# Performance work log

Measured on AMD Instinct MI355X. Metric: run time of the kernel, lower is better.

The kernel has to match this reference:

```python
import jax, jax.numpy as jnp
import numpy as np

B, S, H, I, SI, E, TOPK = 2, 1024, 1024, 512, 2048, 8, 2


def setup_inputs() -> dict:
    key = jax.random.key(0)
    ks = jax.random.split(key, 8)
    w = 0.02
    return {
        "hidden_states": jax.random.normal(ks[0], (B, S, H), jnp.float32),
        "router_weight": jax.random.normal(ks[1], (E, H), jnp.float32) * w,
        "gate_up_proj": jax.random.normal(ks[2], (E, 2 * I, H), jnp.float32) * w,
        "down_proj": jax.random.normal(ks[3], (E, H, I), jnp.float32) * w,
        "shared_gate_w": jax.random.normal(ks[4], (SI, H), jnp.float32) * w,
        "shared_up_w": jax.random.normal(ks[5], (SI, H), jnp.float32) * w,
        "shared_down_w": jax.random.normal(ks[6], (H, SI), jnp.float32) * w,
        "shared_expert_gate_w": jax.random.normal(ks[7], (1, H), jnp.float32) * w,
    }


def reference(hidden_states, router_weight, gate_up_proj, down_proj,
              shared_gate_w, shared_up_w, shared_down_w, shared_expert_gate_w):
    b, s, h = hidden_states.shape
    x = hidden_states.reshape(-1, h)  # [T, H]

    # shared expert (SwiGLU)
    shared = (jax.nn.silu(x @ shared_gate_w.T) * (x @ shared_up_w.T)) @ shared_down_w.T  # [T, H]

    # top-k softmax router (softmax in fp32, renormalized top-k weights)
    logits = x @ router_weight.T  # [T, E]
    probs = jax.nn.softmax(logits.astype(jnp.float32), axis=-1)
    top_v, top_i = jax.lax.top_k(probs, TOPK)
    top_v = (top_v / jnp.sum(top_v, axis=-1, keepdims=True)).astype(logits.dtype)  # [T, K]

    # combine weights per (token, expert): sum over k of routing weight * one_hot
    cw = jnp.sum(jax.nn.one_hot(top_i, E, dtype=top_v.dtype) * top_v[..., None], axis=1)  # [T, E]

    # grouped-expert SwiGLU (dense compute, masked combine == gather/scatter math)
    gu = jnp.einsum('th,eih->eti', x, gate_up_proj)  # [E, T, 2I]
    gate, up = jnp.split(gu, 2, axis=-1)
    act = jax.nn.silu(gate) * up  # [E, T, I]
    per_expert = jnp.einsum('eti,ehi->eth', act, down_proj)  # [E, T, H]
    expert_out = jnp.einsum('eth,te->th', per_expert, cw)  # [T, H]

    out = expert_out + jax.nn.sigmoid(x @ shared_expert_gate_w.T) * shared
    return out.reshape(b, s, h)
```

## Files before the change

kernel.cpp:

```cpp
#include <hip/hip_runtime.h>

#define T_TOK 2048
#define H_DIM 1024
#define I_DIM 512
#define SI_DIM 2048
#define E_NUM 8
#define NSLOT 4096

typedef __attribute__((ext_vector_type(8))) short short8;
typedef __attribute__((ext_vector_type(4))) float floatx4;

__device__ inline unsigned short f2bf(float f) {
  unsigned u = __builtin_bit_cast(unsigned, f);
  u = (u + 0x7FFFu + ((u >> 16) & 1u)) >> 16;
  return (unsigned short)u;
}
__device__ inline float bf2f(unsigned short u) {
  return __builtin_bit_cast(float, (unsigned)u << 16);
}

__device__ inline void gl_lds16(const void* g, void* l) {
  __builtin_amdgcn_global_load_lds(
      (const __attribute__((address_space(1))) unsigned int*)g,
      (__attribute__((address_space(3))) unsigned int*)l, 16, 0, 0);
}

__global__ __launch_bounds__(256) void cast_router(
    const float* __restrict__ x, const float* __restrict__ rw,
    const float* __restrict__ segw,
    const float* __restrict__ s1, const float* __restrict__ s2,
    const float* __restrict__ s3, const float* __restrict__ s4,
    const float* __restrict__ s5,
    unsigned short* __restrict__ d0, unsigned short* __restrict__ d1,
    unsigned short* __restrict__ d2, unsigned short* __restrict__ d3,
    unsigned short* __restrict__ d4, unsigned short* __restrict__ d5,
    int* __restrict__ top2, float2* __restrict__ w01, float* __restrict__ sg) {
  const int bid = blockIdx.x;
  if (bid < 512) {
    int t = bid * 4 + (threadIdx.x >> 6);
    int lane = threadIdx.x & 63;
    const float* xt = x + (long)t * H_DIM;
    float xv[16];
#pragma unroll
    for (int j = 0; j < 16; ++j) xv[j] = xt[j * 64 + lane];
    float dots[9];
#pragma unroll
    for (int e = 0; e < 8; ++e) {
      const float* w = rw + e * H_DIM;
      float s = 0.f;
#pragma unroll
      for (int j = 0; j < 16; ++j) s += xv[j] * w[j * 64 + lane];
      dots[e] = s;
    }
    {
      float s = 0.f;
#pragma unroll
      for (int j = 0; j < 16; ++j) s += xv[j] * segw[j * 64 + lane];
      dots[8] = s;
    }
#pragma unroll
    for (int off = 32; off > 0; off >>= 1) {
#pragma unroll
      for (int e = 0; e < 9; ++e) dots[e] += __shfl_xor(dots[e], off, 64);
    }
    if (lane == 0) {
      int e0 = 0;
      for (int e = 1; e < 8; ++e)
        if (dots[e] > dots[e0]) e0 = e;
      int e1 = (e0 == 0) ? 1 : 0;
      for (int e = 0; e < 8; ++e)
        if (e != e0 && dots[e] > dots[e1]) e1 = e;
      float p1 = expf(dots[e1] - dots[e0]);
      top2[t] = e0 | (e1 << 8);
      w01[t] = make_float2(1.f / (1.f + p1), p1 / (1.f + p1));
      sg[t] = 1.f / (1.f + expf(-dots[8]));
    }
  } else {
    long g = (long)(bid - 512) * 256 + threadIdx.x;
    const float* s;
    unsigned short* d;
    long off;
    if (g < 524288L)       { s = x;  d = d0; off = g; }
    else if (g < 2621440L) { s = s1; d = d1; off = g - 524288L; }
    else if (g < 3670016L) { s = s2; d = d2; off = g - 2621440L; }
    else if (g < 4194304L) { s = s3; d = d3; off = g - 3670016L; }
    else if (g < 4718592L) { s = s4; d = d4; off = g - 4194304L; }
    else                   { s = s5; d = d5; off = g - 4718592L; }
    float4 v = ((const float4*)s)[off];
    ushort4 o;
    o.x = f2bf(v.x); o.y = f2bf(v.y); o.z = f2bf(v.z); o.w = f2bf(v.w);
    ((ushort4*)d)[off] = o;
  }
}

__global__ __launch_bounds__(256) void build_lists(
    const int* __restrict__ top2, int* __restrict__ cnt, int* __restrict__ ebase,
    int* __restrict__ slot_token, int* __restrict__ tok_slot) {
  const int e = blockIdx.x;
  const int tid = threadIdx.x;
  const int lane = tid & 63, wid = tid >> 6;
  __shared__ int wsum[4], wbelow[4];
  const int base_t = tid * 8;
  int mk[8], kk[8];
  int c = 0, below = 0;
#pragma unroll
  for (int j = 0; j < 8; ++j) {
    int p = top2[base_t + j];
    int e0 = p & 0xFF, e1 = (p >> 8) & 0xFF;
    below += (e0 < e) + (e1 < e);
    int m = 0, k = 0;
    if (e0 == e) { m = 1; k = 0; }
    else if (e1 == e) { m = 1; k = 1; }
    mk[j] = m; kk[j] = k;
    c += m;
  }
  int inc = c;
#pragma unroll
  for (int off = 1; off < 64; off <<= 1) {
    int n = __shfl_up(inc, off, 64);
    if (lane >= off) inc += n;
  }
  int bsum = below;
#pragma unroll
  for (int off = 32; off > 0; off >>= 1) bsum += __shfl_xor(bsum, off, 64);
  if (lane == 63) wsum[wid] = inc;
  if (lane == 0) wbelow[wid] = bsum;
  __syncthreads();
  int woff = 0;
#pragma unroll
  for (int i = 0; i < 4; ++i)
    if (i < wid) woff += wsum[i];
  int baseE = wbelow[0] + wbelow[1] + wbelow[2] + wbelow[3];
  int pos = baseE + woff + inc - c;
#pragma unroll
  for (int j = 0; j < 8; ++j) {
    if (mk[j]) {
      slot_token[pos] = base_t + j;
      tok_slot[2 * (base_t + j) + kk[j]] = pos;
      pos++;
    }
  }
  if (tid == 255) cnt[e] = woff + inc;
  if (tid == 0) ebase[e] = baseE;
}

template <bool GATHER>
__device__ __forceinline__ void swiglu_body(
    char* smem, int bx, int by, int e,
    const unsigned short* __restrict__ A, const unsigned short* __restrict__ Bg,
    const unsigned short* __restrict__ Bu, unsigned short* __restrict__ Out,
    const int* __restrict__ slot_token, const int* __restrict__ cnt,
    const int* __restrict__ ebase, int N, int K, long estrideB) {
  constexpr int BM = 128, BN = 128, BK = 32;
  constexpr int ATILE = BM * BK;
  constexpr int BTILE = BN * BK;
  const int tid = threadIdx.x;
  const int lane = tid & 63;
  const int wid = tid >> 6;
  const int wm = wid & 1;
  const int wn = wid >> 1;
  const int m0 = by * BM;
  const int n0 = bx * BN;
  int Meff = 0, baseE = 0;
  if (GATHER) {
    Meff = cnt[e];
    if (m0 >= Meff) return;
    baseE = ebase[e];
  }
  const unsigned short* BgE = Bg + (long)e * estrideB;
  const unsigned short* BuE = Bu + (long)e * estrideB;

  unsigned short* As = (unsigned short*)smem;
  unsigned short* Bgs = As + 2 * ATILE;
  unsigned short* Bus = Bgs + 2 * BTILE;

  const int lrow = lane >> 2;
  const int lcol = (((lane & 3) ^ ((lrow >> 1) & 3)) << 4);

  const char* aP[2];
  const char* bgP[2];
  const char* buP[2];
#pragma unroll
  for (int i = 0; i < 2; ++i) {
    int m = m0 + wid * 32 + i * 16 + lrow;
    long row;
    if (GATHER) {
      int mm = (m < Meff - 1) ? m : (Meff - 1);
      row = slot_token[baseE + mm];
    } else {
      row = m;
    }
    aP[i] = (const char*)A + row * (long)(K * 2) + lcol;
    int n = n0 + wid * 32 + i * 16 + lrow;
    bgP[i] = (const char*)BgE + (long)n * (K * 2) + lcol;
    buP[i] = (const char*)BuE + (long)n * (K * 2) + lcol;
  }

  floatx4 accG[4][4], accU[4][4];
  floatx4 zero = {0.f, 0.f, 0.f, 0.f};
#pragma unroll
  for (int i = 0; i < 4; ++i)
#pragma unroll
    for (int j = 0; j < 4; ++j) { accG[i][j] = zero; accU[i][j] = zero; }

  const int ar = lane & 15;
  const int aksw = (((lane >> 4) ^ ((ar >> 1) & 3)) << 3);

  auto stage = [&](int p, int k0) {
#pragma unroll
    for (int i = 0; i < 2; ++i) {
      gl_lds16(aP[i] + (long)k0 * 2, &As[p * ATILE + (wid * 32 + i * 16) * BK]);
      gl_lds16(bgP[i] + (long)k0 * 2, &Bgs[p * BTILE + (wid * 32 + i * 16) * BK]);
      gl_lds16(buP[i] + (long)k0 * 2, &Bus[p * BTILE + (wid * 32 + i * 16) * BK]);
    }
  };

  stage(0, 0);
  const int NI = K / BK;
  for (int i = 0; i < NI; ++i) {
    __syncthreads();
    if (i + 1 < NI) stage((i + 1) & 1, (i + 1) * BK);
    const unsigned short* Ab = &As[(i & 1) * ATILE];
    const unsigned short* Gb = &Bgs[(i & 1) * BTILE];
    const unsigned short* Ub = &Bus[(i & 1) * BTILE];
    short8 af[4], bgf[4], buf2[4];
#pragma unroll
    for (int tm = 0; tm < 4; ++tm)
      af[tm] = *(const short8*)&Ab[(wm * 64 + tm * 16 + ar) * BK + aksw];
#pragma unroll
    for (int tn = 0; tn < 4; ++tn) {
      bgf[tn] = *(const short8*)&Gb[(wn * 64 + tn * 16 + ar) * BK + aksw];
      buf2[tn] = *(const short8*)&Ub[(wn * 64 + tn * 16 + ar) * BK + aksw];
    }
#pragma unroll
    for (int tm = 0; tm < 4; ++tm)
#pragma unroll
      for (int tn = 0; tn < 4; ++tn) {
        accG[tm][tn] = __builtin_amdgcn_mfma_f32_16x16x32_bf16(af[tm], bgf[tn], accG[tm][tn], 0, 0, 0);
        accU[tm][tn] = __builtin_amdgcn_mfma_f32_16x16x32_bf16(af[tm], buf2[tn], accU[tm][tn], 0, 0, 0);
      }
  }

#pragma unroll
  for (int tm = 0; tm < 4; ++tm)
#pragma unroll
    for (int tn = 0; tn < 4; ++tn)
#pragma unroll
      for (int r = 0; r < 4; ++r) {
        int row = m0 + wm * 64 + tm * 16 + (lane >> 4) * 4 + r;
        int col = n0 + wn * 64 + tn * 16 + (lane & 15);
        if (!GATHER || row < Meff) {
          float g = accG[tm][tn][r];
          float u = accU[tm][tn][r];
          float act = g / (1.f + expf(-g)) * u;
          Out[(long)(baseE + row) * N + col] = f2bf(act);
        }
      }
}

__global__ __launch_bounds__(256, 2) void swiglu_fused(
    const unsigned short* __restrict__ xb, const unsigned short* __restrict__ sgate,
    const unsigned short* __restrict__ sup, unsigned short* __restrict__ act_s,
    const unsigned short* __restrict__ gup, unsigned short* __restrict__ act_e,
    const int* __restrict__ slot_token, const int* __restrict__ cnt,
    const int* __restrict__ ebase) {
  __shared__ __align__(16) char smem[49152];
  int bid = blockIdx.x;
  if (bid < 256) {
    swiglu_body<false>(smem, bid & 15, bid >> 4, 0, xb, sgate, sup, act_s,
                       nullptr, nullptr, nullptr, SI_DIM, H_DIM, 0);
  } else {
    int b2 = bid - 256;
    int e = b2 >> 6;
    int rem = b2 & 63;
    swiglu_body<true>(smem, rem & 3, rem >> 2, e, xb, gup,
                      gup + (long)I_DIM * H_DIM, act_e, slot_token, cnt,
                      ebase, I_DIM, H_DIM, (long)2 * I_DIM * H_DIM);
  }
}

template <int MODE>
__device__ __forceinline__ void down_body(
    char* smem, int bx, int by, int e,
    const unsigned short* __restrict__ A, const unsigned short* __restrict__ B,
    float* __restrict__ OutF, unsigned short* __restrict__ OutB,
    const int* __restrict__ ebase, const int* __restrict__ cnt,
    int N, int Kstride, int kbeg, int kcnt, long estrideB) {
  constexpr int BM = 128, BN = 256, BK = 32;
  constexpr int ATILE = BM * BK;
  constexpr int BTILE = BN * BK;
  const int tid = threadIdx.x;
  const int lane = tid & 63;
  const int wid = tid >> 6;
  const int wm = wid & 1;
  const int wn = wid >> 1;
  const int m0 = by * BM;
  const int n0 = bx * BN;
  int Meff = 0, baseE = 0;
  if (MODE == 1) {
    Meff = cnt[e];
    if (m0 >= Meff) return;
    baseE = ebase[e];
  }
  const unsigned short* BE = B + (long)e * estrideB;

  unsigned short* As = (unsigned short*)smem;
  unsigned short* Bs = As + 2 * ATILE;

  const int lrow = lane >> 2;
  const int lcol = (((lane & 3) ^ ((lrow >> 1) & 3)) << 4);

  const char* aP[2];
  const char* bP[4];
#pragma unroll
  for (int i = 0; i < 2; ++i) {
    int m = m0 + wid * 32 + i * 16 + lrow;
    long arow;
    if (MODE == 1) {
      int mm = (m < Meff - 1) ? m : (Meff - 1);
      arow = baseE + mm;
    } else {
      arow = m;
    }
    aP[i] = (const char*)A + arow * (long)(Kstride * 2) + (long)kbeg * 2 + lcol;
  }
#pragma unroll
  for (int i = 0; i < 4; ++i) {
    int n = n0 + wid * 64 + i * 16 + lrow;
    bP[i] = (const char*)BE + (long)n * (Kstride * 2) + (long)kbeg * 2 + lcol;
  }

  floatx4 acc[4][8];
  floatx4 zero = {0.f, 0.f, 0.f, 0.f};
#pragma unroll
  for (int i = 0; i < 4; ++i)
#pragma unroll
    for (int j = 0; j < 8; ++j) acc[i][j] = zero;

  const int ar = lane & 15;
  const int aksw = (((lane >> 4) ^ ((ar >> 1) & 3)) << 3);

  auto stage = [&](int p, int k0) {
#pragma unroll
    for (int i = 0; i < 2; ++i)
      gl_lds16(aP[i] + (long)k0 * 2, &As[p * ATILE + (wid * 32 + i * 16) * BK]);
#pragma unroll
    for (int i = 0; i < 4; ++i)
      gl_lds16(bP[i] + (long)k0 * 2, &Bs[p * BTILE + (wid * 64 + i * 16) * BK]);
  };

  stage(0, 0);
  const int NI = kcnt / BK;
  for (int i = 0; i < NI; ++i) {
    __syncthreads();
    if (i + 1 < NI) stage((i + 1) & 1, (i + 1) * BK);
    const unsigned short* Ab = &As[(i & 1) * ATILE];
    const unsigned short* Bb = &Bs[(i & 1) * BTILE];
    short8 af[4], bf[8];
#pragma unroll
    for (int tm = 0; tm < 4; ++tm)
      af[tm] = *(const short8*)&Ab[(wm * 64 + tm * 16 + ar) * BK + aksw];
#pragma unroll
    for (int tn = 0; tn < 8; ++tn)
      bf[tn] = *(const short8*)&Bb[(wn * 128 + tn * 16 + ar) * BK + aksw];
#pragma unroll
    for (int tm = 0; tm < 4; ++tm)
#pragma unroll
      for (int tn = 0; tn < 8; ++tn)
        acc[tm][tn] = __builtin_amdgcn_mfma_f32_16x16x32_bf16(af[tm], bf[tn], acc[tm][tn], 0, 0, 0);
  }

#pragma unroll
  for (int tm = 0; tm < 4; ++tm)
#pragma unroll
    for (int r = 0; r < 4; ++r) {
      int row = m0 + wm * 64 + tm * 16 + (lane >> 4) * 4 + r;
#pragma unroll
      for (int tn = 0; tn < 8; ++tn) {
        int col = n0 + wn * 128 + tn * 16 + (lane & 15);
        float v = acc[tm][tn][r];
        if (MODE == 0) {
          OutF[(long)row * N + col] = v;
        } else if (MODE == 2) {
          OutB[(long)row * N + col] = f2bf(v);
        } else if (row < Meff) {
          OutB[(long)(baseE + row) * N + col] = f2bf(v);
        }
      }
    }
}

__global__ __launch_bounds__(256, 2) void down_fused(
    const unsigned short* __restrict__ act_s, const unsigned short* __restrict__ sdown,
    float* __restrict__ out, unsigned short* __restrict__ spart,
    const unsigned short* __restrict__ act_e, const unsigned short* __restrict__ downw,
    unsigned short* __restrict__ eout, const int* __restrict__ ebase,
    const int* __restrict__ cnt) {
  __shared__ __align__(16) char smem[49152];
  int bid = blockIdx.x;
  if (bid < 128) {
    int ks = bid >> 6;
    int rem = bid & 63;
    if (ks == 0)
      down_body<0>(smem, rem & 3, rem >> 2, 0, act_s, sdown, out, nullptr,
                   nullptr, nullptr, H_DIM, SI_DIM, 0, 1024, 0);
    else
      down_body<2>(smem, rem & 3, rem >> 2, 0, act_s, sdown, nullptr, spart,
                   nullptr, nullptr, H_DIM, SI_DIM, 1024, 1024, 0);
  } else {
    int b2 = bid - 128;
    int e = b2 >> 6;
    int rem = b2 & 63;
    down_body<1>(smem, rem & 3, rem >> 2, e, act_e, downw, nullptr, eout,
                 ebase, cnt, H_DIM, I_DIM, 0, I_DIM, (long)H_DIM * I_DIM);
  }
}

__global__ __launch_bounds__(256) void combine_kernel(
    float* __restrict__ out, const unsigned short* __restrict__ spart,
    const unsigned short* __restrict__ eout, const float* __restrict__ sg,
    const float2* __restrict__ w01, const int* __restrict__ tok_slot) {
  int t = blockIdx.x;
  int c = threadIdx.x;
  float sgr = sg[t];
  float2 wr = w01[t];
  int s0 = tok_slot[2 * t];
  int s1 = tok_slot[2 * t + 1];
  ushort4 p1 = ((const ushort4*)(spart + (long)t * H_DIM))[c];
  ushort4 e0 = ((const ushort4*)(eout + (long)s0 * H_DIM))[c];
  ushort4 e1 = ((const ushort4*)(eout + (long)s1 * H_DIM))[c];
  float4* op = &((float4*)(out + (long)t * H_DIM))[c];
  float4 o = *op;
  o.x = sgr * (o.x + bf2f(p1.x)) + wr.x * bf2f(e0.x) + wr.y * bf2f(e1.x);
  o.y = sgr * (o.y + bf2f(p1.y)) + wr.x * bf2f(e0.y) + wr.y * bf2f(e1.y);
  o.z = sgr * (o.z + bf2f(p1.z)) + wr.x * bf2f(e0.z) + wr.y * bf2f(e1.z);
  o.w = sgr * (o.w + bf2f(p1.w)) + wr.x * bf2f(e0.w) + wr.y * bf2f(e1.w);
  *op = o;
}

extern "C" void kernel_launch(void* const* d_in, const int* in_sizes, int n_in,
                              void* d_out, int out_size, void* d_ws, size_t ws_size,
                              hipStream_t stream) {
  const float* x = (const float*)d_in[0];
  const float* rw = (const float*)d_in[1];
  const float* gup = (const float*)d_in[2];
  const float* dwn = (const float*)d_in[3];
  const float* sgw = (const float*)d_in[4];
  const float* suw = (const float*)d_in[5];
  const float* sdw = (const float*)d_in[6];
  const float* segw = (const float*)d_in[7];
  float* out = (float*)d_out;

  char* w = (char*)d_ws;
  unsigned short* xb = (unsigned short*)(w + 0);
  unsigned short* gup_b = (unsigned short*)(w + 4194304L);
  unsigned short* down_b = (unsigned short*)(w + 20971520L);
  unsigned short* sgate_b = (unsigned short*)(w + 29360128L);
  unsigned short* sup_b = (unsigned short*)(w + 33554432L);
  unsigned short* sdown_b = (unsigned short*)(w + 37748736L);
  unsigned short* act_s = (unsigned short*)(w + 41943040L);
  unsigned short* act_e = (unsigned short*)(w + 50331648L);
  unsigned short* eout = (unsigned short*)(w + 54525952L);
  float* sg = (float*)(w + 62914560L);
  int* top2 = (int*)(w + 62922752L);
  float2* w01 = (float2*)(w + 62930944L);
  int* cnt = (int*)(w + 62947328L);
  int* ebase = (int*)(w + 62947584L);
  int* slot_token = (int*)(w + 62947840L);
  int* tok_slot = (int*)(w + 62964224L);
  unsigned short* spart = xb;

  cast_router<<<20992, 256, 0, stream>>>(x, rw, segw, gup, dwn, sgw, suw, sdw,
                                         xb, gup_b, down_b, sgate_b, sup_b,
                                         sdown_b, top2, w01, sg);
  build_lists<<<E_NUM, 256, 0, stream>>>(top2, cnt, ebase, slot_token, tok_slot);
  swiglu_fused<<<768, 256, 0, stream>>>(xb, sgate_b, sup_b, act_s, gup_b,
                                        act_e, slot_token, cnt, ebase);
  down_fused<<<640, 256, 0, stream>>>(act_s, sdown_b, out, spart, act_e,
                                      down_b, eout, ebase, cnt);
  combine_kernel<<<T_TOK, 256, 0, stream>>>(out, spart, eout, sg, w01, tok_slot);
}
```

Before: 200.2 us.

## Fuse combine into down GEMM epilogue via scaled atomicAdd into zeroed output

Removes the separate combine kernel and the bf16 intermediate buffers for the shared split-K partial and the per-expert outputs. The down GEMM epilogues now scale by the sigmoid gate or the routing weight and atomically add into the fp32 output, which the cast kernel zeroes first. The cast kernel also handles 8 elements per thread, so fewer blocks are launched. The trade is about 4 fp32 atomic adds per output element, which contend in L2, and a summation order that is no longer deterministic.

```diff
diff --git a/kernel.cpp b/kernel.cpp
--- a/kernel.cpp
+++ b/kernel.cpp
@@ -34,6 +34,7 @@
     unsigned short* __restrict__ d0, unsigned short* __restrict__ d1,
     unsigned short* __restrict__ d2, unsigned short* __restrict__ d3,
     unsigned short* __restrict__ d4, unsigned short* __restrict__ d5,
+    float* __restrict__ outz,
     int* __restrict__ top2, float2* __restrict__ w01, float* __restrict__ sg) {
   const int bid = blockIdx.x;
   if (bid < 512) {
@@ -75,27 +76,39 @@
       w01[t] = make_float2(1.f / (1.f + p1), p1 / (1.f + p1));
       sg[t] = 1.f / (1.f + expf(-dots[8]));
     }
-  } else {
+  } else if (bid < 10752) {
     long g = (long)(bid - 512) * 256 + threadIdx.x;
     const float* s;
     unsigned short* d;
     long off;
-    if (g < 524288L)       { s = x;  d = d0; off = g; }
-    else if (g < 2621440L) { s = s1; d = d1; off = g - 524288L; }
-    else if (g < 3670016L) { s = s2; d = d2; off = g - 2621440L; }
-    else if (g < 4194304L) { s = s3; d = d3; off = g - 3670016L; }
-    else if (g < 4718592L) { s = s4; d = d4; off = g - 4194304L; }
-    else                   { s = s5; d = d5; off = g - 4718592L; }
-    float4 v = ((const float4*)s)[off];
-    ushort4 o;
-    o.x = f2bf(v.x); o.y = f2bf(v.y); o.z = f2bf(v.z); o.w = f2bf(v.w);
-    ((ushort4*)d)[off] = o;
+    if (g < 262144L)        { s = x;  d = d0; off = g; }
+    else if (g < 1310720L)  { s = s1; d = d1; off = g - 262144L; }
+    else if (g < 1835008L)  { s = s2; d = d2; off = g - 1310720L; }
+    else if (g < 2097152L)  { s = s3; d = d3; off = g - 1835008L; }
+    else if (g < 2359296L)  { s = s4; d = d4; off = g - 2097152L; }
+    else                    { s = s5; d = d5; off = g - 2359296L; }
+    const float4* sp = (const float4*)s;
+    float4 v0 = sp[off * 2];
+    float4 v1 = sp[off * 2 + 1];
+    uint4 u;
+    u.x = (unsigned)f2bf(v0.x) | ((unsigned)f2bf(v0.y) << 16);
+    u.y = (unsigned)f2bf(v0.z) | ((unsigned)f2bf(v0.w) << 16);
+    u.z = (unsigned)f2bf(v1.x) | ((unsigned)f2bf(v1.y) << 16);
+    u.w = (unsigned)f2bf(v1.z) | ((unsigned)f2bf(v1.w) << 16);
+    ((uint4*)d)[off] = u;
+  } else {
+    long zi = (long)(bid - 10752) * 256 + threadIdx.x;
+    float4 z = {0.f, 0.f, 0.f, 0.f};
+    float4* o4 = (float4*)outz;
+    o4[zi * 2] = z;
+    o4[zi * 2 + 1] = z;
   }
 }
 
 __global__ __launch_bounds__(256) void build_lists(
-    const int* __restrict__ top2, int* __restrict__ cnt, int* __restrict__ ebase,
-    int* __restrict__ slot_token, int* __restrict__ tok_slot) {
+    const int* __restrict__ top2, const float2* __restrict__ w01,
+    int* __restrict__ cnt, int* __restrict__ ebase,
+    int* __restrict__ slot_token, float* __restrict__ swt) {
   const int e = blockIdx.x;
   const int tid = threadIdx.x;
   const int lane = tid & 63, wid = tid >> 6;
@@ -135,8 +148,10 @@
 #pragma unroll
   for (int j = 0; j < 8; ++j) {
     if (mk[j]) {
-      slot_token[pos] = base_t + j;
-      tok_slot[2 * (base_t + j) + kk[j]] = pos;
+      int t = base_t + j;
+      slot_token[pos] = t;
+      float2 wr = w01[t];
+      swt[pos] = kk[j] ? wr.y : wr.x;
       pos++;
     }
   }
@@ -283,7 +298,9 @@
 __device__ __forceinline__ void down_body(
     char* smem, int bx, int by, int e,
     const unsigned short* __restrict__ A, const unsigned short* __restrict__ B,
-    float* __restrict__ OutF, unsigned short* __restrict__ OutB,
+    float* __restrict__ out,
+    const float* __restrict__ sg, const float* __restrict__ swt,
+    const int* __restrict__ slot_token,
     const int* __restrict__ ebase, const int* __restrict__ cnt,
     int N, int Kstride, int kbeg, int kcnt, long estrideB) {
   constexpr int BM = 128, BN = 256, BK = 32;
@@ -375,67 +392,47 @@
 #pragma unroll
     for (int r = 0; r < 4; ++r) {
       int row = m0 + wm * 64 + tm * 16 + (lane >> 4) * 4 + r;
+      if (MODE == 1 && row >= Meff) continue;
+      float sc;
+      long trow;
+      if (MODE == 0) {
+        sc = sg[row];
+        trow = row;
+      } else {
+        sc = swt[baseE + row];
+        trow = slot_token[baseE + row];
+      }
+      float* orow = out + trow * (long)N;
 #pragma unroll
       for (int tn = 0; tn < 8; ++tn) {
         int col = n0 + wn * 128 + tn * 16 + (lane & 15);
-        float v = acc[tm][tn][r];
-        if (MODE == 0) {
-          OutF[(long)row * N + col] = v;
-        } else if (MODE == 2) {
-          OutB[(long)row * N + col] = f2bf(v);
-        } else if (row < Meff) {
-          OutB[(long)(baseE + row) * N + col] = f2bf(v);
-        }
+        atomicAdd(&orow[col], sc * acc[tm][tn][r]);
       }
     }
 }
 
 __global__ __launch_bounds__(256, 2) void down_fused(
     const unsigned short* __restrict__ act_s, const unsigned short* __restrict__ sdown,
-    float* __restrict__ out, unsigned short* __restrict__ spart,
+    float* __restrict__ out,
     const unsigned short* __restrict__ act_e, const unsigned short* __restrict__ downw,
-    unsigned short* __restrict__ eout, const int* __restrict__ ebase,
-    const int* __restrict__ cnt) {
+    const float* __restrict__ sg, const float* __restrict__ swt,
+    const int* __restrict__ slot_token,
+    const int* __restrict__ ebase, const int* __restrict__ cnt) {
   __shared__ __align__(16) char smem[49152];
   int bid = blockIdx.x;
   if (bid < 128) {
     int ks = bid >> 6;
     int rem = bid & 63;
-    if (ks == 0)
-      down_body<0>(smem, rem & 3, rem >> 2, 0, act_s, sdown, out, nullptr,
-                   nullptr, nullptr, H_DIM, SI_DIM, 0, 1024, 0);
-    else
-      down_body<2>(smem, rem & 3, rem >> 2, 0, act_s, sdown, nullptr, spart,
-                   nullptr, nullptr, H_DIM, SI_DIM, 1024, 1024, 0);
+    down_body<0>(smem, rem & 3, rem >> 2, 0, act_s, sdown, out, sg, nullptr,
+                 nullptr, nullptr, nullptr, H_DIM, SI_DIM, ks * 1024, 1024, 0);
   } else {
     int b2 = bid - 128;
     int e = b2 >> 6;
     int rem = b2 & 63;
-    down_body<1>(smem, rem & 3, rem >> 2, e, act_e, downw, nullptr, eout,
-                 ebase, cnt, H_DIM, I_DIM, 0, I_DIM, (long)H_DIM * I_DIM);
-  }
-}
-
-__global__ __launch_bounds__(256) void combine_kernel(
-    float* __restrict__ out, const unsigned short* __restrict__ spart,
-    const unsigned short* __restrict__ eout, const float* __restrict__ sg,
-    const float2* __restrict__ w01, const int* __restrict__ tok_slot) {
-  int t = blockIdx.x;
-  int c = threadIdx.x;
-  float sgr = sg[t];
-  float2 wr = w01[t];
-  int s0 = tok_slot[2 * t];
-  int s1 = tok_slot[2 * t + 1];
-  ushort4 p1 = ((const ushort4*)(spart + (long)t * H_DIM))[c];
-  ushort4 e0 = ((const ushort4*)(eout + (long)s0 * H_DIM))[c];
-  ushort4 e1 = ((const ushort4*)(eout + (long)s1 * H_DIM))[c];
-  float4* op = &((float4*)(out + (long)t * H_DIM))[c];
-  float4 o = *op;
-  o.x = sgr * (o.x + bf2f(p1.x)) + wr.x * bf2f(e0.x) + wr.y * bf2f(e1.x);
-  o.y = sgr * (o.y + bf2f(p1.y)) + wr.x * bf2f(e0.y) + wr.y * bf2f(e1.y);
-  o.z = sgr * (o.z + bf2f(p1.z)) + wr.x * bf2f(e0.z) + wr.y * bf2f(e1.z);
-  o.w = sgr * (o.w + bf2f(p1.w)) + wr.x * bf2f(e0.w) + wr.y * bf2f(e1.w);
-  *op = o;
+    down_body<1>(smem, rem & 3, rem >> 2, e, act_e, downw, out, nullptr, swt,
+                 slot_token, ebase, cnt, H_DIM, I_DIM, 0, I_DIM,
+                 (long)H_DIM * I_DIM);
+  }
 }
 
 extern "C" void kernel_launch(void* const* d_in, const int* in_sizes, int n_in,
@@ -460,23 +457,20 @@
   unsigned short* sdown_b = (unsigned short*)(w + 37748736L);
   unsigned short* act_s = (unsigned short*)(w + 41943040L);
   unsigned short* act_e = (unsigned short*)(w + 50331648L);
-  unsigned short* eout = (unsigned short*)(w + 54525952L);
+  float* swt = (float*)(w + 54525952L);
   float* sg = (float*)(w + 62914560L);
   int* top2 = (int*)(w + 62922752L);
   float2* w01 = (float2*)(w + 62930944L);
   int* cnt = (int*)(w + 62947328L);
   int* ebase = (int*)(w + 62947584L);
   int* slot_token = (int*)(w + 62947840L);
-  int* tok_slot = (int*)(w + 62964224L);
-  unsigned short* spart = xb;
-
-  cast_router<<<20992, 256, 0, stream>>>(x, rw, segw, gup, dwn, sgw, suw, sdw,
+
+  cast_router<<<11776, 256, 0, stream>>>(x, rw, segw, gup, dwn, sgw, suw, sdw,
                                          xb, gup_b, down_b, sgate_b, sup_b,
-                                         sdown_b, top2, w01, sg);
-  build_lists<<<E_NUM, 256, 0, stream>>>(top2, cnt, ebase, slot_token, tok_slot);
+                                         sdown_b, out, top2, w01, sg);
+  build_lists<<<E_NUM, 256, 0, stream>>>(top2, w01, cnt, ebase, slot_token, swt);
   swiglu_fused<<<768, 256, 0, stream>>>(xb, sgate_b, sup_b, act_s, gup_b,
                                         act_e, slot_token, cnt, ebase);
-  down_fused<<<640, 256, 0, stream>>>(act_s, sdown_b, out, spart, act_e,
-                                      down_b, eout, ebase, cnt);
-  combine_kernel<<<T_TOK, 256, 0, stream>>>(out, spart, eout, sg, w01, tok_slot);
-}
+  down_fused<<<640, 256, 0, stream>>>(act_s, sdown_b, out, act_e, down_b,
+                                      sg, swt, slot_token, ebase, cnt);
+}
```

New measurement: 214.3 us. 7.1% more time.
